# Kernel optimization log

Measured on AMD Instinct MI355X. Metric: run time of the kernel, lower is better.

The kernel has to match this reference:

```python
import jax, jax.numpy as jnp
import numpy as np

D_MODEL = 1024
NUM_HEADS = 16
D_K = D_MODEL // NUM_HEADS
THETA = 10000.0


def apply_rope(x, positions):
    # x: [b, h, s, d_k]; positions: [b, s] int32
    half = D_K // 2
    inv_freq = THETA ** (-jnp.arange(half, dtype=jnp.float32) * 2.0 / D_K)  # [half]
    angles = positions[:, None, :, None].astype(jnp.float32) * inv_freq  # [b,1,s,half]
    cos, sin = jnp.cos(angles), jnp.sin(angles)
    x1 = x[..., 0::2]  # even dims
    x2 = x[..., 1::2]  # odd dims
    out_even = x1 * cos - x2 * sin
    out_odd = x1 * sin + x2 * cos
    # re-interleave
    out = jnp.stack([out_even, out_odd], axis=-1)
    return out.reshape(x.shape)


def setup_inputs() -> dict:
    key = jax.random.key(0)
    ks = jax.random.split(key, 5)
    b, s = 2, 2048
    scale = 0.02
    return {
        "x": jax.random.normal(ks[0], (b, s, D_MODEL), dtype=jnp.float32),
        "Wq": jax.random.normal(ks[1], (D_MODEL, D_MODEL), dtype=jnp.float32) * scale,
        "Wk": jax.random.normal(ks[2], (D_MODEL, D_MODEL), dtype=jnp.float32) * scale,
        "Wv": jax.random.normal(ks[3], (D_MODEL, D_MODEL), dtype=jnp.float32) * scale,
        "Wo": jax.random.normal(ks[4], (D_MODEL, D_MODEL), dtype=jnp.float32) * scale,
    }


def reference(x, Wq, Wk, Wv, Wo):
    b, s, _ = x.shape
    # Linear(d, d) applied as x @ W^T (torch Linear convention, no bias)
    Q = x @ Wq.T
    K = x @ Wk.T
    V = x @ Wv.T
    # split heads: [b, s, h*d] -> [b, h, s, d]
    split = lambda t: t.reshape(b, s, NUM_HEADS, D_K).transpose(0, 2, 1, 3)
    Q, K, V = split(Q), split(K), split(V)
    positions = jnp.broadcast_to(jnp.arange(s, dtype=jnp.int32), (b, s))
    Q = apply_rope(Q, positions)
    K = apply_rope(K, positions)
    scores = jnp.einsum('bhqd,bhkd->bhqk', Q, K) / jnp.sqrt(jnp.float32(D_K))
    causal = jnp.tril(jnp.ones((s, s), dtype=bool))
    scores = jnp.where(causal[None, None], scores, -jnp.inf)
    attn = jax.nn.softmax(scores, axis=-1)
    out = jnp.einsum('bhqk,bhkd->bhqd', attn, V)
    out = out.transpose(0, 2, 1, 3).reshape(b, s, D_MODEL)
    return out @ Wo.T
```

## Files before the change

### kernel.cpp

```cpp
#include <hip/hip_runtime.h>

typedef __attribute__((ext_vector_type(8))) short bf16x8;
typedef __attribute__((ext_vector_type(4))) float f32x4;
typedef __attribute__((ext_vector_type(16))) float f32x16;

typedef const __attribute__((address_space(1))) unsigned int gu32;
typedef __attribute__((address_space(3))) unsigned int lu32;

__device__ __forceinline__ void async16(const void* g, void* l) {
  __builtin_amdgcn_global_load_lds((gu32*)g, (lu32*)l, 16, 0, 0);
}

__device__ __forceinline__ unsigned short f2bf(float f) {
  unsigned int u = __float_as_uint(f);
  u += 0x7fffu + ((u >> 16) & 1u);
  return (unsigned short)(u >> 16);
}
__device__ __forceinline__ float b2f(unsigned short s) {
  return __uint_as_float(((unsigned int)s) << 16);
}
__device__ __forceinline__ unsigned int cvtpk(float lo, float hi) {
  unsigned int w;
  asm("v_cvt_pk_bf16_f32 %0, %1, %2" : "=v"(w) : "v"(lo), "v"(hi));
  return w;
}
__device__ __forceinline__ void plswap(unsigned int& x, unsigned int& y) {
  asm("v_permlane32_swap_b32 %0, %1" : "+v"(x), "+v"(y));
}

__global__ __launch_bounds__(256) void cvt_k(const float* __restrict__ in,
                                             unsigned short* __restrict__ out,
                                             int n4) {
  int i = blockIdx.x * 256 + threadIdx.x;
  if (i >= n4) return;
  float4 v = ((const float4*)in)[i];
  ushort4 o;
  o.x = f2bf(v.x); o.y = f2bf(v.y); o.z = f2bf(v.z); o.w = f2bf(v.w);
  ((ushort4*)out)[i] = o;
}

template <int WRITE_F32>
__global__ __launch_bounds__(256) void gemm_bt(const unsigned short* __restrict__ A,
                                               const unsigned short* __restrict__ B,
                                               void* __restrict__ Cp, int N, int K) {
  __shared__ __align__(16) unsigned short Al[2][128 * 64];
  __shared__ __align__(16) unsigned short Bl[2][128 * 64];
  const int t = threadIdx.x;
  const int w = t >> 6, l = t & 63;
  const int wm = w >> 1, wn = w & 1;
  const int lr = l & 15, lg = l >> 4;
  const long bm = (long)blockIdx.x * 128, bn = (long)blockIdx.y * 128;
  const int srow = t >> 3;
  const int scol = (t & 7) * 8;
  const int scolS = ((t & 7) ^ (srow & 7)) * 8;
  const int KT = K >> 6;
  f32x4 acc[4][4] = {};

  auto STAGE = [&](int ts) {
    const int bi = ts & 1;
    const int k0 = ts * 64;
    #pragma unroll
    for (int r = 0; r < 4; ++r) {
      int row = r * 32 + srow;
      async16(&A[(bm + row) * (long)K + k0 + scolS], &Al[bi][row * 64 + scol]);
      async16(&B[(bn + row) * (long)K + k0 + scolS], &Bl[bi][row * 64 + scol]);
    }
  };

  STAGE(0);
  for (int kt = 0; kt < KT; ++kt) {
    const int cur = kt & 1;
    asm volatile("s_waitcnt vmcnt(0)" ::: "memory");
    __builtin_amdgcn_s_barrier();
    __builtin_amdgcn_sched_barrier(0);
    if (kt + 1 < KT) STAGE(kt + 1);
    #pragma unroll
    for (int ks = 0; ks < 2; ++ks) {
      const int slot = ((ks * 4 + lg) ^ (lr & 7)) * 8;
      bf16x8 af[4], bf[4];
      #pragma unroll
      for (int i = 0; i < 4; ++i) {
        af[i] = *(const bf16x8*)&Al[cur][(wm * 64 + i * 16 + lr) * 64 + slot];
        bf[i] = *(const bf16x8*)&Bl[cur][(wn * 64 + i * 16 + lr) * 64 + slot];
      }
      #pragma unroll
      for (int i = 0; i < 4; ++i)
        #pragma unroll
        for (int j = 0; j < 4; ++j)
          acc[i][j] = __builtin_amdgcn_mfma_f32_16x16x32_bf16(af[i], bf[j], acc[i][j], 0, 0, 0);
    }
  }
  #pragma unroll
  for (int i = 0; i < 4; ++i)
    #pragma unroll
    for (int j = 0; j < 4; ++j)
      #pragma unroll
      for (int r = 0; r < 4; ++r) {
        long row = bm + wm * 64 + i * 16 + lg * 4 + r;
        long col = bn + wn * 64 + j * 16 + lr;
        float v = acc[i][j][r];
        if (WRITE_F32) ((float*)Cp)[row * N + col] = v;
        else ((unsigned short*)Cp)[row * N + col] = f2bf(v);
      }
}

__global__ __launch_bounds__(256) void rope_k(unsigned short* __restrict__ QKV) {
  int idx = blockIdx.x * 256 + threadIdx.x;
  int row = idx >> 9;
  int rem = idx & 511;
  int h = rem >> 5;
  int i = rem & 31;
  int s = row & 2047;
  float invf = exp2f((float)i * (-13.287712379549449f / 32.0f));
  float ang = (float)s * invf;
  float sn, cs;
  sincosf(ang, &sn, &cs);
  size_t base = (size_t)row * 3072 + h * 64 + 2 * i;
  #pragma unroll
  for (int qk = 0; qk < 2; ++qk) {
    size_t off = base + (size_t)qk * 1024;
    float x1 = b2f(QKV[off]);
    float x2 = b2f(QKV[off + 1]);
    QKV[off]     = f2bf(x1 * cs - x2 * sn);
    QKV[off + 1] = f2bf(x1 * sn + x2 * cs);
  }
}

__global__ __launch_bounds__(256) void vtr_k(const unsigned short* __restrict__ QKV,
                                             unsigned short* __restrict__ Vt) {
  __shared__ unsigned short tl[64][66];
  const int kt = blockIdx.x;
  const int bh = blockIdx.y;
  const int b = bh >> 4, h = bh & 15;
  const int t = threadIdx.x;
  const int row = t >> 3, c8 = t & 7;
  #pragma unroll
  for (int r = 0; r < 2; ++r) {
    int k = r * 32 + row;
    bf16x8 v = *(const bf16x8*)&QKV[((long)b * 2048 + kt * 64 + k) * 3072 + 2048 + h * 64 + c8 * 8];
    #pragma unroll
    for (int j = 0; j < 8; ++j) tl[c8 * 8 + j][k] = (unsigned short)v[j];
  }
  __syncthreads();
  #pragma unroll
  for (int r = 0; r < 2; ++r) {
    int d = r * 32 + row;
    ushort4 a, bq;
    a.x = tl[d][c8 * 8 + 0]; a.y = tl[d][c8 * 8 + 1];
    a.z = tl[d][c8 * 8 + 2]; a.w = tl[d][c8 * 8 + 3];
    bq.x = tl[d][c8 * 8 + 4]; bq.y = tl[d][c8 * 8 + 5];
    bq.z = tl[d][c8 * 8 + 6]; bq.w = tl[d][c8 * 8 + 7];
    long off = ((long)bh * 64 + d) * 2048 + kt * 64 + c8 * 8;
    *(ushort4*)&Vt[off] = a;
    *(ushort4*)&Vt[off + 4] = bq;
  }
}

__global__ __launch_bounds__(128) void attn_k(const unsigned short* __restrict__ QKV,
                                              const unsigned short* __restrict__ VtG,
                                              unsigned short* __restrict__ O) {
  __shared__ __align__(16) unsigned short Kl[3][64 * 64];
  __shared__ __align__(16) unsigned short Vl[3][64 * 64];
  const int t = threadIdx.x;
  const int w = t >> 6, l = t & 63;
  const int q31 = l & 31, hi = l >> 5;
  const int bh = blockIdx.x;
  const int qt = 31 - (int)blockIdx.y;
  const int b = bh >> 4, h = bh & 15;
  const int Qb = qt * 64;
  const long rowb = (long)b * 2048;
  const int L = 3072;
  const int NT = qt + 1;
  const int srow = t >> 3;
  const int scol = (t & 7) * 8;
  const int scolK = ((t & 7) ^ (srow & 7)) * 8;
  const float cexp = 0.125f * 1.4426950408889634f;

  const int qmy = Qb + 32 * w + q31;
  const long qgrow = rowb + qmy;

  bf16x8 qf[4];
  #pragma unroll
  for (int dk = 0; dk < 4; ++dk)
    qf[dk] = *(const bf16x8*)&QKV[qgrow * L + h * 64 + dk * 16 + hi * 8];

  float m_ = -1e30f, ls = 0.0f;
  f32x16 oa[2];
  #pragma unroll
  for (int dt = 0; dt < 2; ++dt)
    #pragma unroll
    for (int r = 0; r < 16; ++r) oa[dt][r] = 0.0f;

  auto STAGE = [&](int ts) {
    const int bi = ts % 3;
    const long kb = rowb + (long)ts * 64;
    const long vrowb = (long)bh * 64;
    #pragma unroll
    for (int r = 0; r < 4; ++r) {
      int row = r * 16 + srow;
      async16(&QKV[(kb + row) * L + 1024 + h * 64 + scolK], &Kl[bi][row * 64 + scol]);
      async16(&VtG[(vrowb + row) * 2048 + ts * 64 + scolK], &Vl[bi][row * 64 + scol]);
    }
  };

  STAGE(0);
  if (NT > 1) STAGE(1);

  for (int kt = 0; kt < NT; ++kt) {
    const int cur = kt % 3;
    if (kt < NT - 1) asm volatile("s_waitcnt vmcnt(8)" ::: "memory");
    else             asm volatile("s_waitcnt vmcnt(0)" ::: "memory");
    __builtin_amdgcn_s_barrier();
    __builtin_amdgcn_sched_barrier(0);
    if (kt + 2 < NT) STAGE(kt + 2);

    f32x16 st[2];
    #pragma unroll
    for (int kt2 = 0; kt2 < 2; ++kt2)
      #pragma unroll
      for (int r = 0; r < 16; ++r) st[kt2][r] = 0.0f;
    __builtin_amdgcn_s_setprio(1);
    #pragma unroll
    for (int dk = 0; dk < 4; ++dk)
      #pragma unroll
      for (int kt2 = 0; kt2 < 2; ++kt2) {
        int krow = kt2 * 32 + q31;
        bf16x8 kfr = *(const bf16x8*)&Kl[cur][krow * 64 + (((2 * dk + hi) ^ (krow & 7)) * 8)];
        st[kt2] = __builtin_amdgcn_mfma_f32_32x32x16_bf16(kfr, qf[dk], st[kt2], 0, 0, 0);
      }
    __builtin_amdgcn_s_setprio(0);
    if (kt == NT - 1) {
      #pragma unroll
      for (int kt2 = 0; kt2 < 2; ++kt2)
        #pragma unroll
        for (int r = 0; r < 16; ++r) {
          int kg = kt * 64 + kt2 * 32 + (r & 3) + 8 * (r >> 2) + 4 * hi;
          if (kg > qmy) st[kt2][r] = -1e30f;
        }
    }
    float m0[8];
    #pragma unroll
    for (int i = 0; i < 8; ++i)
      m0[i] = fmaxf(fmaxf(st[0][i], st[0][i + 8]), fmaxf(st[1][i], st[1][i + 8]));
    float mt = fmaxf(fmaxf(fmaxf(m0[0], m0[1]), fmaxf(m0[2], m0[3])),
                     fmaxf(fmaxf(m0[4], m0[5]), fmaxf(m0[6], m0[7])));
    mt = fmaxf(mt, __shfl_xor(mt, 32, 64));
    if (__any((mt - m_) * cexp > 8.0f)) {
      float mn = fmaxf(m_, mt);
      float al = __builtin_amdgcn_exp2f((m_ - mn) * cexp);
      m_ = mn;
      ls *= al;
      #pragma unroll
      for (int dt = 0; dt < 2; ++dt)
        #pragma unroll
        for (int r = 0; r < 16; ++r) oa[dt][r] *= al;
    }
    const float mc = m_ * cexp;
    #pragma unroll
    for (int kt2 = 0; kt2 < 2; ++kt2)
      #pragma unroll
      for (int r = 0; r < 16; ++r)
        st[kt2][r] = __builtin_amdgcn_exp2f(fmaf(st[kt2][r], cexp, -mc));
    float s0[8];
    #pragma unroll
    for (int i = 0; i < 8; ++i)
      s0[i] = (st[0][i] + st[0][i + 8]) + (st[1][i] + st[1][i + 8]);
    float rs = ((s0[0] + s0[1]) + (s0[2] + s0[3])) + ((s0[4] + s0[5]) + (s0[6] + s0[7]));
    rs += __shfl_xor(rs, 32, 64);
    ls += rs;
    bf16x8 pfr[4];
    #pragma unroll
    for (int ks = 0; ks < 4; ++ks) {
      int tt = ks >> 1, gX = 2 * (ks & 1), gY = gX + 1;
      unsigned int x1 = cvtpk(st[tt][4 * gX + 0], st[tt][4 * gX + 1]);
      unsigned int y1 = cvtpk(st[tt][4 * gY + 0], st[tt][4 * gY + 1]);
      plswap(x1, y1);
      unsigned int x2 = cvtpk(st[tt][4 * gX + 2], st[tt][4 * gX + 3]);
      unsigned int y2 = cvtpk(st[tt][4 * gY + 2], st[tt][4 * gY + 3]);
      plswap(x2, y2);
      union { unsigned int u[4]; bf16x8 b; } cc;
      cc.u[0] = x1; cc.u[1] = x2; cc.u[2] = y1; cc.u[3] = y2;
      pfr[ks] = cc.b;
    }
    __builtin_amdgcn_s_setprio(1);
    #pragma unroll
    for (int dt = 0; dt < 2; ++dt)
      #pragma unroll
      for (int ks = 0; ks < 4; ++ks) {
        int vrow = dt * 32 + q31;
        bf16x8 vf = *(const bf16x8*)&Vl[cur][vrow * 64 + (((2 * ks + hi) ^ (vrow & 7)) * 8)];
        oa[dt] = __builtin_amdgcn_mfma_f32_32x32x16_bf16(vf, pfr[ks], oa[dt], 0, 0, 0);
      }
    __builtin_amdgcn_s_setprio(0);
  }
  float inv = 1.0f / ls;
  #pragma unroll
  for (int dt = 0; dt < 2; ++dt)
    #pragma unroll
    for (int g = 0; g < 4; ++g) {
      ushort4 o4;
      o4.x = f2bf(oa[dt][4 * g + 0] * inv);
      o4.y = f2bf(oa[dt][4 * g + 1] * inv);
      o4.z = f2bf(oa[dt][4 * g + 2] * inv);
      o4.w = f2bf(oa[dt][4 * g + 3] * inv);
      *(ushort4*)&O[qgrow * 1024 + h * 64 + dt * 32 + 8 * g + 4 * hi] = o4;
    }
}

extern "C" void kernel_launch(void* const* d_in, const int* in_sizes, int n_in,
                              void* d_out, int out_size, void* d_ws, size_t ws_size,
                              hipStream_t stream) {
  const float* x  = (const float*)d_in[0];
  const float* Wq = (const float*)d_in[1];
  const float* Wk = (const float*)d_in[2];
  const float* Wv = (const float*)d_in[3];
  const float* Wo = (const float*)d_in[4];
  char* ws = (char*)d_ws;
  unsigned short* xb   = (unsigned short*)(ws);
  unsigned short* Wb   = (unsigned short*)(ws + (8u << 20));
  unsigned short* Wob  = (unsigned short*)(ws + (14u << 20));
  unsigned short* QKVb = (unsigned short*)(ws + (16u << 20));
  unsigned short* Ob   = (unsigned short*)(ws + (40u << 20));
  unsigned short* Vtg  = xb;

  cvt_k<<<4096, 256, 0, stream>>>(x, xb, 4096 * 1024 / 4);
  cvt_k<<<1024, 256, 0, stream>>>(Wq, Wb, 1024 * 1024 / 4);
  cvt_k<<<1024, 256, 0, stream>>>(Wk, Wb + 1024 * 1024, 1024 * 1024 / 4);
  cvt_k<<<1024, 256, 0, stream>>>(Wv, Wb + 2 * 1024 * 1024, 1024 * 1024 / 4);
  cvt_k<<<1024, 256, 0, stream>>>(Wo, Wob, 1024 * 1024 / 4);

  gemm_bt<0><<<dim3(32, 24), 256, 0, stream>>>(xb, Wb, QKVb, 3072, 1024);
  rope_k<<<(4096 * 512) / 256, 256, 0, stream>>>(QKVb);
  vtr_k<<<dim3(32, 32), 256, 0, stream>>>(QKVb, Vtg);
  attn_k<<<dim3(32, 32), 128, 0, stream>>>(QKVb, Vtg, Ob);
  gemm_bt<1><<<dim3(32, 8), 256, 0, stream>>>(Ob, Wob, d_out, 1024, 1024);
}
```

Measured before the change: 137.4 us.

## Shrink GEMM K-tile, vectorize RoPE per row, and double-buffer attention

The GEMM K-tile drops from 64 to 32 and loses the XOR swizzle on its shared-memory layout, which halves LDS use but doubles the barrier count and can add bank conflicts. RoPE now runs one block per row: 32 threads compute sin/cos once into shared memory and every thread rotates 8 bf16 values with vector loads and stores, replacing scalar strided accesses and the repeated sincos per element. Attention goes from triple to double buffering with a full vmcnt(0) wait, and the cross-half row-sum shuffle is deferred to the end of the loop. This reduces LDS and shuffles but gives less prefetch overlap.

```diff
diff --git a/kernel.cpp b/kernel.cpp
--- a/kernel.cpp
+++ b/kernel.cpp
@@ -43,27 +43,26 @@
 __global__ __launch_bounds__(256) void gemm_bt(const unsigned short* __restrict__ A,
                                                const unsigned short* __restrict__ B,
                                                void* __restrict__ Cp, int N, int K) {
-  __shared__ __align__(16) unsigned short Al[2][128 * 64];
-  __shared__ __align__(16) unsigned short Bl[2][128 * 64];
+  __shared__ __align__(16) unsigned short Al[2][128 * 32];
+  __shared__ __align__(16) unsigned short Bl[2][128 * 32];
   const int t = threadIdx.x;
   const int w = t >> 6, l = t & 63;
   const int wm = w >> 1, wn = w & 1;
   const int lr = l & 15, lg = l >> 4;
   const long bm = (long)blockIdx.x * 128, bn = (long)blockIdx.y * 128;
-  const int srow = t >> 3;
-  const int scol = (t & 7) * 8;
-  const int scolS = ((t & 7) ^ (srow & 7)) * 8;
-  const int KT = K >> 6;
+  const int srow = t >> 2;
+  const int c8 = t & 3;
+  const int KT = K >> 5;
   f32x4 acc[4][4] = {};
 
   auto STAGE = [&](int ts) {
     const int bi = ts & 1;
-    const int k0 = ts * 64;
-    #pragma unroll
-    for (int r = 0; r < 4; ++r) {
-      int row = r * 32 + srow;
-      async16(&A[(bm + row) * (long)K + k0 + scolS], &Al[bi][row * 64 + scol]);
-      async16(&B[(bn + row) * (long)K + k0 + scolS], &Bl[bi][row * 64 + scol]);
+    const int k0 = ts * 32;
+    #pragma unroll
+    for (int r = 0; r < 2; ++r) {
+      int row = r * 64 + srow;
+      async16(&A[(bm + row) * (long)K + k0 + c8 * 8], &Al[bi][row * 32 + c8 * 8]);
+      async16(&B[(bn + row) * (long)K + k0 + c8 * 8], &Bl[bi][row * 32 + c8 * 8]);
     }
   };
 
@@ -74,21 +73,17 @@
     __builtin_amdgcn_s_barrier();
     __builtin_amdgcn_sched_barrier(0);
     if (kt + 1 < KT) STAGE(kt + 1);
-    #pragma unroll
-    for (int ks = 0; ks < 2; ++ks) {
-      const int slot = ((ks * 4 + lg) ^ (lr & 7)) * 8;
-      bf16x8 af[4], bf[4];
-      #pragma unroll
-      for (int i = 0; i < 4; ++i) {
-        af[i] = *(const bf16x8*)&Al[cur][(wm * 64 + i * 16 + lr) * 64 + slot];
-        bf[i] = *(const bf16x8*)&Bl[cur][(wn * 64 + i * 16 + lr) * 64 + slot];
-      }
-      #pragma unroll
-      for (int i = 0; i < 4; ++i)
-        #pragma unroll
-        for (int j = 0; j < 4; ++j)
-          acc[i][j] = __builtin_amdgcn_mfma_f32_16x16x32_bf16(af[i], bf[j], acc[i][j], 0, 0, 0);
-    }
+    bf16x8 af[4], bf[4];
+    #pragma unroll
+    for (int i = 0; i < 4; ++i) {
+      af[i] = *(const bf16x8*)&Al[cur][(wm * 64 + i * 16 + lr) * 32 + lg * 8];
+      bf[i] = *(const bf16x8*)&Bl[cur][(wn * 64 + i * 16 + lr) * 32 + lg * 8];
+    }
+    #pragma unroll
+    for (int i = 0; i < 4; ++i)
+      #pragma unroll
+      for (int j = 0; j < 4; ++j)
+        acc[i][j] = __builtin_amdgcn_mfma_f32_16x16x32_bf16(af[i], bf[j], acc[i][j], 0, 0, 0);
   }
   #pragma unroll
   for (int i = 0; i < 4; ++i)
@@ -105,25 +100,31 @@
 }
 
 __global__ __launch_bounds__(256) void rope_k(unsigned short* __restrict__ QKV) {
-  int idx = blockIdx.x * 256 + threadIdx.x;
-  int row = idx >> 9;
-  int rem = idx & 511;
-  int h = rem >> 5;
-  int i = rem & 31;
-  int s = row & 2047;
-  float invf = exp2f((float)i * (-13.287712379549449f / 32.0f));
-  float ang = (float)s * invf;
-  float sn, cs;
-  sincosf(ang, &sn, &cs);
-  size_t base = (size_t)row * 3072 + h * 64 + 2 * i;
-  #pragma unroll
-  for (int qk = 0; qk < 2; ++qk) {
-    size_t off = base + (size_t)qk * 1024;
-    float x1 = b2f(QKV[off]);
-    float x2 = b2f(QKV[off + 1]);
-    QKV[off]     = f2bf(x1 * cs - x2 * sn);
-    QKV[off + 1] = f2bf(x1 * sn + x2 * cs);
-  }
+  __shared__ float csl[32], snl[32];
+  const int row = blockIdx.x;
+  const int s = row & 2047;
+  const int t = threadIdx.x;
+  if (t < 32) {
+    float invf = exp2f((float)t * (-13.287712379549449f / 32.0f));
+    float sn, cs;
+    sincosf((float)s * invf, &sn, &cs);
+    csl[t] = cs; snl[t] = sn;
+  }
+  __syncthreads();
+  const int col0 = (t < 128) ? t * 8 : 1024 + (t - 128) * 8;
+  const int i0 = (t & 7) * 4;
+  unsigned short* p = &QKV[(size_t)row * 3072 + col0];
+  bf16x8 v = *(const bf16x8*)p;
+  bf16x8 o;
+  #pragma unroll
+  for (int j = 0; j < 4; ++j) {
+    float x1 = b2f((unsigned short)v[2 * j]);
+    float x2 = b2f((unsigned short)v[2 * j + 1]);
+    float cs = csl[i0 + j], sn = snl[i0 + j];
+    o[2 * j]     = (short)f2bf(x1 * cs - x2 * sn);
+    o[2 * j + 1] = (short)f2bf(x1 * sn + x2 * cs);
+  }
+  *(bf16x8*)p = o;
 }
 
 __global__ __launch_bounds__(256) void vtr_k(const unsigned short* __restrict__ QKV,
@@ -159,8 +160,8 @@
 __global__ __launch_bounds__(128) void attn_k(const unsigned short* __restrict__ QKV,
                                               const unsigned short* __restrict__ VtG,
                                               unsigned short* __restrict__ O) {
-  __shared__ __align__(16) unsigned short Kl[3][64 * 64];
-  __shared__ __align__(16) unsigned short Vl[3][64 * 64];
+  __shared__ __align__(16) unsigned short Kl[2][64 * 64];
+  __shared__ __align__(16) unsigned short Vl[2][64 * 64];
   const int t = threadIdx.x;
   const int w = t >> 6, l = t & 63;
   const int q31 = l & 31, hi = l >> 5;
@@ -192,7 +193,7 @@
     for (int r = 0; r < 16; ++r) oa[dt][r] = 0.0f;
 
   auto STAGE = [&](int ts) {
-    const int bi = ts % 3;
+    const int bi = ts & 1;
     const long kb = rowb + (long)ts * 64;
     const long vrowb = (long)bh * 64;
     #pragma unroll
@@ -204,15 +205,13 @@
   };
 
   STAGE(0);
-  if (NT > 1) STAGE(1);
 
   for (int kt = 0; kt < NT; ++kt) {
-    const int cur = kt % 3;
-    if (kt < NT - 1) asm volatile("s_waitcnt vmcnt(8)" ::: "memory");
-    else             asm volatile("s_waitcnt vmcnt(0)" ::: "memory");
+    const int cur = kt & 1;
+    asm volatile("s_waitcnt vmcnt(0)" ::: "memory");
     __builtin_amdgcn_s_barrier();
     __builtin_amdgcn_sched_barrier(0);
-    if (kt + 2 < NT) STAGE(kt + 2);
+    if (kt + 1 < NT) STAGE(kt + 1);
 
     f32x16 st[2];
     #pragma unroll
@@ -244,9 +243,9 @@
       m0[i] = fmaxf(fmaxf(st[0][i], st[0][i + 8]), fmaxf(st[1][i], st[1][i + 8]));
     float mt = fmaxf(fmaxf(fmaxf(m0[0], m0[1]), fmaxf(m0[2], m0[3])),
                      fmaxf(fmaxf(m0[4], m0[5]), fmaxf(m0[6], m0[7])));
-    mt = fmaxf(mt, __shfl_xor(mt, 32, 64));
     if (__any((mt - m_) * cexp > 8.0f)) {
-      float mn = fmaxf(m_, mt);
+      float mg = fmaxf(mt, __shfl_xor(mt, 32, 64));
+      float mn = fmaxf(m_, mg);
       float al = __builtin_amdgcn_exp2f((m_ - mn) * cexp);
       m_ = mn;
       ls *= al;
@@ -265,9 +264,7 @@
     #pragma unroll
     for (int i = 0; i < 8; ++i)
       s0[i] = (st[0][i] + st[0][i + 8]) + (st[1][i] + st[1][i + 8]);
-    float rs = ((s0[0] + s0[1]) + (s0[2] + s0[3])) + ((s0[4] + s0[5]) + (s0[6] + s0[7]));
-    rs += __shfl_xor(rs, 32, 64);
-    ls += rs;
+    ls += ((s0[0] + s0[1]) + (s0[2] + s0[3])) + ((s0[4] + s0[5]) + (s0[6] + s0[7]));
     bf16x8 pfr[4];
     #pragma unroll
     for (int ks = 0; ks < 4; ++ks) {
@@ -293,7 +290,8 @@
       }
     __builtin_amdgcn_s_setprio(0);
   }
-  float inv = 1.0f / ls;
+  float lt = ls + __shfl_xor(ls, 32, 64);
+  float inv = 1.0f / lt;
   #pragma unroll
   for (int dt = 0; dt < 2; ++dt)
     #pragma unroll
@@ -330,7 +328,7 @@
   cvt_k<<<1024, 256, 0, stream>>>(Wo, Wob, 1024 * 1024 / 4);
 
   gemm_bt<0><<<dim3(32, 24), 256, 0, stream>>>(xb, Wb, QKVb, 3072, 1024);
-  rope_k<<<(4096 * 512) / 256, 256, 0, stream>>>(QKVb);
+  rope_k<<<4096, 256, 0, stream>>>(QKVb);
   vtr_k<<<dim3(32, 32), 256, 0, stream>>>(QKVb, Vtg);
   attn_k<<<dim3(32, 32), 128, 0, stream>>>(QKVb, Vtg, Ob);
   gemm_bt<1><<<dim3(32, 8), 256, 0, stream>>>(Ob, Wob, d_out, 1024, 1024);
```

Measured after the change: 133.7 us. 1.03x faster.
